# Kernel tuning notes

Measured on AMD Instinct MI355X. Metric: run time of the kernel, lower is better.

The kernel has to match this reference:

```python
import jax, jax.numpy as jnp
import numpy as np


def sparsemax(z):
    """Euclidean projection onto the simplex (Martins & Astudillo 2016).
    z: (..., L) logits -> sparse probability vectors of same shape.
    """
    L = z.shape[-1]
    z_sorted = jnp.flip(jnp.sort(z, axis=-1), axis=-1)          # descending
    cum = jnp.cumsum(z_sorted, axis=-1)
    k = jnp.arange(1, L + 1, dtype=z.dtype)                     # 1..L
    support = 1.0 + k * z_sorted > cum                          # prefix-true mask
    k_max = jnp.sum(support, axis=-1, keepdims=True).astype(z.dtype)
    # sum of z_sorted over the support == cumsum at the last supported index
    cum_at_k = jnp.sum(jnp.where(support, z_sorted, 0.0), axis=-1, keepdims=True)
    tau = (cum_at_k - 1.0) / k_max
    return jnp.maximum(z - tau, 0.0)


def setup_inputs() -> dict:
    key = jax.random.key(0)
    k1, k2 = jax.random.split(key)
    B, K, L = 64, 16, 16384
    attention_logits = jax.random.normal(k1, (B, K, L), dtype=jnp.float32)
    rationale_mask = (jax.random.uniform(k2, (B, L)) < 0.1).astype(jnp.float32)
    return {"attention_logits": attention_logits, "rationale_mask": rationale_mask}


def reference(attention_logits, rationale_mask):
    # normalize the rationale mask into a probability target q
    q = rationale_mask / jnp.clip(
        jnp.sum(rationale_mask, axis=-1, keepdims=True), 1e-12, None
    )  # (B, L)
    p = sparsemax(attention_logits)            # (B, K, L), all heads batched
    diff = p - q[:, None, :]                   # broadcast target over heads
    # per-(example, head) loss 0.5*||p - q||^2, then mean over batch and heads
    # (= mean over heads of per-head batch means, as in the torch loop)
    return 0.5 * jnp.mean(jnp.sum(diff * diff, axis=-1))
```

## Files before the change

### kernel.cpp

```cpp
#include <hip/hip_runtime.h>

#define BB 64
#define KK 16
#define LL 16384
#define CAP 2048

__global__ __launch_bounds__(256) void mask_stats_kernel(
    const float* __restrict__ mask, float* __restrict__ stats) {
  int b = blockIdx.x;
  const float* m = mask + (size_t)b * LL;
  int t = threadIdx.x;
  float s = 0.f, sq = 0.f;
#pragma unroll
  for (int j = 0; j < 16; ++j) {
    float4 v = reinterpret_cast<const float4*>(m)[j * 256 + t];
    s  += v.x + v.y + v.z + v.w;
    sq += v.x * v.x + v.y * v.y + v.z * v.z + v.w * v.w;
  }
  for (int off = 32; off; off >>= 1) {
    s  += __shfl_xor(s, off);
    sq += __shfl_xor(sq, off);
  }
  __shared__ float ls[4], lsq[4];
  int wave = t >> 6;
  if ((t & 63) == 0) { ls[wave] = s; lsq[wave] = sq; }
  __syncthreads();
  if (t == 0) {
    float S  = ls[0] + ls[1] + ls[2] + ls[3];
    float SQ = lsq[0] + lsq[1] + lsq[2] + lsq[3];
    float inv = 1.0f / fmaxf(S, 1e-12f);
    stats[2 * b]     = inv;
    stats[2 * b + 1] = SQ * inv * inv;
  }
}

__global__ __launch_bounds__(256) void sparsemax_loss_kernel(
    const float* __restrict__ logits, const float* __restrict__ mask,
    const float* __restrict__ stats, float* __restrict__ out) {
  int row = blockIdx.x;
  int b = row >> 4;
  const float* z = logits + (size_t)row * LL;
  const float* m = mask + (size_t)b * LL;
  int t = threadIdx.x;
  int wave = t >> 6, lane = t & 63;

  __shared__ float lds_val[CAP];
  __shared__ int   lds_idx[CAP];
  __shared__ int   lds_n;
  __shared__ float lds_f[4];

  if (t == 0) lds_n = 0;

  float4 v[16];
  float vmax = -3.0e38f;
#pragma unroll
  for (int j = 0; j < 16; ++j) {
    v[j] = reinterpret_cast<const float4*>(z)[j * 256 + t];
    vmax = fmaxf(vmax, fmaxf(fmaxf(v[j].x, v[j].y), fmaxf(v[j].z, v[j].w)));
  }
  for (int off = 32; off; off >>= 1) vmax = fmaxf(vmax, __shfl_xor(vmax, off));
  if (lane == 0) lds_f[wave] = vmax;
  __syncthreads();
  float zmax = fmaxf(fmaxf(lds_f[0], lds_f[1]), fmaxf(lds_f[2], lds_f[3]));
  float thr = zmax - 1.0f;

#pragma unroll
  for (int j = 0; j < 16; ++j) {
    int base = (j * 256 + t) * 4;
    float vv[4] = {v[j].x, v[j].y, v[j].z, v[j].w};
#pragma unroll
    for (int e = 0; e < 4; ++e) {
      if (vv[e] > thr) {
        int pos = atomicAdd(&lds_n, 1);
        if (pos < CAP) { lds_val[pos] = vv[e]; lds_idx[pos] = base + e; }
      }
    }
  }
  __syncthreads();
  int n = lds_n;
  float inv_s = stats[2 * b];
  float sumq2 = stats[2 * b + 1];
  const float scale = 0.5f / (float)(BB * KK);

  if (n <= 64) {
    if (wave == 0) {
      float c = (lane < n) ? lds_val[lane] : -3.0e38f;
#pragma unroll
      for (int size = 2; size <= 64; size <<= 1) {
#pragma unroll
        for (int stride = size >> 1; stride > 0; stride >>= 1) {
          float other = __shfl_xor(c, stride);
          bool dirDesc = ((lane & size) == 0);
          bool takeMax = (dirDesc == ((lane & stride) == 0));
          float mn = fminf(c, other), mx = fmaxf(c, other);
          c = takeMax ? mx : mn;
        }
      }
      float cum = c;
#pragma unroll
      for (int off = 1; off < 64; off <<= 1) {
        float y = __shfl_up(cum, off);
        if (lane >= off) cum += y;
      }
      bool sup = (lane < n) && (1.0f + (float)(lane + 1) * c > cum);
      unsigned long long bal = __ballot(sup);
      int k = __popcll(bal);
      float S = sup ? c : 0.f;
      for (int off = 32; off; off >>= 1) S += __shfl_xor(S, off);
      float tau = (S - 1.0f) / (float)k;

      float a1 = 0.f, a2 = 0.f;
      if (lane < n) {
        float val = lds_val[lane];
        float p = fmaxf(val - tau, 0.f);
        if (p > 0.f) {
          float q = m[lds_idx[lane]] * inv_s;
          a1 = p * p;
          a2 = p * q;
        }
      }
      for (int off = 32; off; off >>= 1) {
        a1 += __shfl_xor(a1, off);
        a2 += __shfl_xor(a2, off);
      }
      if (lane == 0) atomicAdd(out, (a1 - 2.f * a2 + sumq2) * scale);
    }
  } else if (n <= CAP) {
    if (wave == 0) {
      int nj = (n + 63) >> 6;
      float lo = thr, hi = zmax;
      for (int it = 0; it < 30; ++it) {
        float mid = 0.5f * (lo + hi);
        float s = 0.f;
        for (int j = 0; j < nj; ++j) {
          int i = j * 64 + lane;
          float cc = (i < n) ? lds_val[i] : -3.0e38f;
          s += fmaxf(cc - mid, 0.f);
        }
        for (int off = 32; off; off >>= 1) s += __shfl_xor(s, off);
        if (s >= 1.0f) lo = mid; else hi = mid;
      }
      float S = 0.f, kc = 0.f;
      for (int j = 0; j < nj; ++j) {
        int i = j * 64 + lane;
        float cc = (i < n) ? lds_val[i] : -3.0e38f;
        if (cc > lo) { S += cc; kc += 1.f; }
      }
      for (int off = 32; off; off >>= 1) {
        S  += __shfl_xor(S, off);
        kc += __shfl_xor(kc, off);
      }
      float tau = (S - 1.0f) / kc;

      float a1 = 0.f, a2 = 0.f;
      for (int j = 0; j < nj; ++j) {
        int i = j * 64 + lane;
        if (i < n) {
          float p = fmaxf(lds_val[i] - tau, 0.f);
          if (p > 0.f) {
            float q = m[lds_idx[i]] * inv_s;
            a1 += p * p;
            a2 += p * q;
          }
        }
      }
      for (int off = 32; off; off >>= 1) {
        a1 += __shfl_xor(a1, off);
        a2 += __shfl_xor(a2, off);
      }
      if (lane == 0) atomicAdd(out, (a1 - 2.f * a2 + sumq2) * scale);
    }
  } else {
    __shared__ float red[4], red2[4];
    float lo = thr, hi = zmax;
    for (int it = 0; it < 30; ++it) {
      float mid = 0.5f * (lo + hi);
      float s = 0.f;
      for (int j = 0; j < 16; ++j) {
        float4 vv = reinterpret_cast<const float4*>(z)[j * 256 + t];
        s += fmaxf(vv.x - mid, 0.f) + fmaxf(vv.y - mid, 0.f) +
             fmaxf(vv.z - mid, 0.f) + fmaxf(vv.w - mid, 0.f);
      }
      for (int off = 32; off; off >>= 1) s += __shfl_xor(s, off);
      __syncthreads();
      if (lane == 0) red[wave] = s;
      __syncthreads();
      float tot = red[0] + red[1] + red[2] + red[3];
      if (tot >= 1.0f) lo = mid; else hi = mid;
    }
    float S = 0.f, kc = 0.f;
    for (int j = 0; j < 16; ++j) {
      float4 vv4 = reinterpret_cast<const float4*>(z)[j * 256 + t];
      float vv[4] = {vv4.x, vv4.y, vv4.z, vv4.w};
      for (int e = 0; e < 4; ++e)
        if (vv[e] > lo) { S += vv[e]; kc += 1.f; }
    }
    for (int off = 32; off; off >>= 1) {
      S  += __shfl_xor(S, off);
      kc += __shfl_xor(kc, off);
    }
    __syncthreads();
    if (lane == 0) { red[wave] = S; red2[wave] = kc; }
    __syncthreads();
    S  = red[0] + red[1] + red[2] + red[3];
    kc = red2[0] + red2[1] + red2[2] + red2[3];
    float tau = (S - 1.0f) / kc;

    float a1 = 0.f, a2 = 0.f;
    for (int j = 0; j < 16; ++j) {
      int base = (j * 256 + t) * 4;
      float4 vv4 = reinterpret_cast<const float4*>(z)[j * 256 + t];
      float vv[4] = {vv4.x, vv4.y, vv4.z, vv4.w};
      for (int e = 0; e < 4; ++e) {
        float p = fmaxf(vv[e] - tau, 0.f);
        if (p > 0.f) {
          float q = m[base + e] * inv_s;
          a1 += p * p;
          a2 += p * q;
        }
      }
    }
    for (int off = 32; off; off >>= 1) {
      a1 += __shfl_xor(a1, off);
      a2 += __shfl_xor(a2, off);
    }
    __syncthreads();
    if (lane == 0) { red[wave] = a1; red2[wave] = a2; }
    __syncthreads();
    if (t == 0) {
      a1 = red[0] + red[1] + red[2] + red[3];
      a2 = red2[0] + red2[1] + red2[2] + red2[3];
      atomicAdd(out, (a1 - 2.f * a2 + sumq2) * scale);
    }
  }
}

extern "C" void kernel_launch(void* const* d_in, const int* in_sizes, int n_in,
                              void* d_out, int out_size, void* d_ws, size_t ws_size,
                              hipStream_t stream) {
  const float* logits = (const float*)d_in[0];
  const float* mask   = (const float*)d_in[1];
  float* stats = (float*)d_ws;
  float* out   = (float*)d_out;

  hipMemsetAsync(out, 0, sizeof(float), stream);
  mask_stats_kernel<<<BB, 256, 0, stream>>>(mask, stats);
  sparsemax_loss_kernel<<<BB * KK, 256, 0, stream>>>(logits, mask, stats, out);
}
```

Before: 111.0 us.

## Split rows into segments across three kernels for rowmax, compaction, and solve

Restructures the single per-row kernel into three passes: a segmented row-max kernel, which also computes the mask stats, using atomicMax on order-preserving keys; a segmented compaction kernel writing candidates to global memory; and a wave-per-row solve kernel. The goal is more blocks for parallelism and latency hiding on the 64MB logits read. In exchange, logits are now read twice from global memory, and it adds extra launches, a memset, and global atomics on per-row counters.

```diff
diff --git a/kernel.cpp b/kernel.cpp
--- a/kernel.cpp
+++ b/kernel.cpp
@@ -3,236 +3,199 @@
 #define BB 64
 #define KK 16
 #define LL 16384
-#define CAP 2048
-
-__global__ __launch_bounds__(256) void mask_stats_kernel(
-    const float* __restrict__ mask, float* __restrict__ stats) {
-  int b = blockIdx.x;
+#define NROW (BB * KK)
+#define SEGS 4
+#define CAP 512
+
+__device__ __forceinline__ unsigned fkey(float f) {
+  unsigned u = __float_as_uint(f);
+  return (u & 0x80000000u) ? ~u : (u | 0x80000000u);
+}
+__device__ __forceinline__ float funkey(unsigned k) {
+  unsigned u = (k & 0x80000000u) ? (k & 0x7fffffffu) : ~k;
+  return __uint_as_float(u);
+}
+
+__global__ __launch_bounds__(256) void k1_rowmax_maskstats(
+    const float* __restrict__ logits, const float* __restrict__ mask,
+    unsigned* __restrict__ rowmax, float* __restrict__ stats) {
+  int gb = blockIdx.x, t = threadIdx.x, wave = t >> 6, lane = t & 63;
+  __shared__ float l0[4], l1[4];
+  if (gb < NROW * SEGS) {
+    int row = gb >> 2, seg = gb & 3;
+    const float4* zv = reinterpret_cast<const float4*>(logits) +
+                       (size_t)row * (LL / 4) + seg * (LL / 4 / SEGS);
+    float4 a = zv[t], b4 = zv[t + 256], c = zv[t + 512], d = zv[t + 768];
+    float m0 = fmaxf(fmaxf(a.x, a.y), fmaxf(a.z, a.w));
+    float m1 = fmaxf(fmaxf(b4.x, b4.y), fmaxf(b4.z, b4.w));
+    float m2 = fmaxf(fmaxf(c.x, c.y), fmaxf(c.z, c.w));
+    float m3 = fmaxf(fmaxf(d.x, d.y), fmaxf(d.z, d.w));
+    float m = fmaxf(fmaxf(m0, m1), fmaxf(m2, m3));
+    for (int off = 32; off; off >>= 1) m = fmaxf(m, __shfl_xor(m, off));
+    if (lane == 0) l0[wave] = m;
+    __syncthreads();
+    if (t == 0) {
+      float bm = fmaxf(fmaxf(l0[0], l0[1]), fmaxf(l0[2], l0[3]));
+      atomicMax(&rowmax[row], fkey(bm));
+    }
+  } else {
+    int b = gb - NROW * SEGS;
+    const float* m = mask + (size_t)b * LL;
+    float s = 0.f, sq = 0.f;
+#pragma unroll
+    for (int j = 0; j < 16; ++j) {
+      float4 v = reinterpret_cast<const float4*>(m)[j * 256 + t];
+      s  += v.x + v.y + v.z + v.w;
+      sq += v.x * v.x + v.y * v.y + v.z * v.z + v.w * v.w;
+    }
+    for (int off = 32; off; off >>= 1) {
+      s += __shfl_xor(s, off); sq += __shfl_xor(sq, off);
+    }
+    if (lane == 0) { l0[wave] = s; l1[wave] = sq; }
+    __syncthreads();
+    if (t == 0) {
+      float S  = l0[0] + l0[1] + l0[2] + l0[3];
+      float SQ = l1[0] + l1[1] + l1[2] + l1[3];
+      float inv = 1.0f / fmaxf(S, 1e-12f);
+      stats[2 * b]     = inv;
+      stats[2 * b + 1] = SQ * inv * inv;
+    }
+  }
+}
+
+__global__ __launch_bounds__(256) void k2_compact(
+    const float* __restrict__ logits, const unsigned* __restrict__ rowmax,
+    int* __restrict__ cnt, float* __restrict__ cval, int* __restrict__ cidx) {
+  int gb = blockIdx.x;
+  int row = gb >> 2, seg = gb & 3;
+  int t = threadIdx.x;
+  float thr = funkey(rowmax[row]) - 1.0f;
+  const float4* zv = reinterpret_cast<const float4*>(logits) +
+                     (size_t)row * (LL / 4) + seg * (LL / 4 / SEGS);
+  float4 a = zv[t], b4 = zv[t + 256], c = zv[t + 512], d = zv[t + 768];
+  int ebase = seg * (LL / SEGS);
+  float vv[16] = {a.x,  a.y,  a.z,  a.w,  b4.x, b4.y, b4.z, b4.w,
+                  c.x,  c.y,  c.z,  c.w,  d.x,  d.y,  d.z,  d.w};
+  float* cv = cval + (size_t)row * CAP;
+  int*   ci = cidx + (size_t)row * CAP;
+#pragma unroll
+  for (int j = 0; j < 16; ++j) {
+    if (vv[j] > thr) {
+      int idx = ebase + (j >> 2) * 1024 + t * 4 + (j & 3);
+      int pos = atomicAdd(&cnt[row], 1);
+      if (pos < CAP) { cv[pos] = vv[j]; ci[pos] = idx; }
+    }
+  }
+}
+
+__global__ __launch_bounds__(256) void k3_solve(
+    const float* __restrict__ logits, const float* __restrict__ mask,
+    const unsigned* __restrict__ rowmax, const int* __restrict__ cnt,
+    const float* __restrict__ cval, const int* __restrict__ cidx,
+    const float* __restrict__ stats, float* __restrict__ out) {
+  int t = threadIdx.x, wave = t >> 6, lane = t & 63;
+  int row = blockIdx.x * 4 + wave;
+  int b = row >> 4;
+  __shared__ float part[4];
+  int n = cnt[row];
+  float zmax = funkey(rowmax[row]);
+  float thr = zmax - 1.0f;
+  float inv_s = stats[2 * b], sumq2 = stats[2 * b + 1];
+  const float scale = 0.5f / (float)(BB * KK);
   const float* m = mask + (size_t)b * LL;
-  int t = threadIdx.x;
-  float s = 0.f, sq = 0.f;
-#pragma unroll
-  for (int j = 0; j < 16; ++j) {
-    float4 v = reinterpret_cast<const float4*>(m)[j * 256 + t];
-    s  += v.x + v.y + v.z + v.w;
-    sq += v.x * v.x + v.y * v.y + v.z * v.z + v.w * v.w;
-  }
-  for (int off = 32; off; off >>= 1) {
-    s  += __shfl_xor(s, off);
-    sq += __shfl_xor(sq, off);
-  }
-  __shared__ float ls[4], lsq[4];
-  int wave = t >> 6;
-  if ((t & 63) == 0) { ls[wave] = s; lsq[wave] = sq; }
-  __syncthreads();
-  if (t == 0) {
-    float S  = ls[0] + ls[1] + ls[2] + ls[3];
-    float SQ = lsq[0] + lsq[1] + lsq[2] + lsq[3];
-    float inv = 1.0f / fmaxf(S, 1e-12f);
-    stats[2 * b]     = inv;
-    stats[2 * b + 1] = SQ * inv * inv;
-  }
-}
-
-__global__ __launch_bounds__(256) void sparsemax_loss_kernel(
-    const float* __restrict__ logits, const float* __restrict__ mask,
-    const float* __restrict__ stats, float* __restrict__ out) {
-  int row = blockIdx.x;
-  int b = row >> 4;
-  const float* z = logits + (size_t)row * LL;
-  const float* m = mask + (size_t)b * LL;
-  int t = threadIdx.x;
-  int wave = t >> 6, lane = t & 63;
-
-  __shared__ float lds_val[CAP];
-  __shared__ int   lds_idx[CAP];
-  __shared__ int   lds_n;
-  __shared__ float lds_f[4];
-
-  if (t == 0) lds_n = 0;
-
-  float4 v[16];
-  float vmax = -3.0e38f;
-#pragma unroll
-  for (int j = 0; j < 16; ++j) {
-    v[j] = reinterpret_cast<const float4*>(z)[j * 256 + t];
-    vmax = fmaxf(vmax, fmaxf(fmaxf(v[j].x, v[j].y), fmaxf(v[j].z, v[j].w)));
-  }
-  for (int off = 32; off; off >>= 1) vmax = fmaxf(vmax, __shfl_xor(vmax, off));
-  if (lane == 0) lds_f[wave] = vmax;
-  __syncthreads();
-  float zmax = fmaxf(fmaxf(lds_f[0], lds_f[1]), fmaxf(lds_f[2], lds_f[3]));
-  float thr = zmax - 1.0f;
-
-#pragma unroll
-  for (int j = 0; j < 16; ++j) {
-    int base = (j * 256 + t) * 4;
-    float vv[4] = {v[j].x, v[j].y, v[j].z, v[j].w};
-#pragma unroll
-    for (int e = 0; e < 4; ++e) {
-      if (vv[e] > thr) {
-        int pos = atomicAdd(&lds_n, 1);
-        if (pos < CAP) { lds_val[pos] = vv[e]; lds_idx[pos] = base + e; }
+  const float* cv = cval + (size_t)row * CAP;
+  const int*   ci = cidx + (size_t)row * CAP;
+  float a1 = 0.f, a2 = 0.f;
+
+  if (n <= 64) {
+    float c = (lane < n) ? cv[lane] : -3.0e38f;
+#pragma unroll
+    for (int size = 2; size <= 64; size <<= 1) {
+#pragma unroll
+      for (int stride = size >> 1; stride > 0; stride >>= 1) {
+        float other = __shfl_xor(c, stride);
+        bool dirDesc = ((lane & size) == 0);
+        bool takeMax = (dirDesc == ((lane & stride) == 0));
+        c = takeMax ? fmaxf(c, other) : fminf(c, other);
       }
     }
-  }
-  __syncthreads();
-  int n = lds_n;
-  float inv_s = stats[2 * b];
-  float sumq2 = stats[2 * b + 1];
-  const float scale = 0.5f / (float)(BB * KK);
-
-  if (n <= 64) {
-    if (wave == 0) {
-      float c = (lane < n) ? lds_val[lane] : -3.0e38f;
-#pragma unroll
-      for (int size = 2; size <= 64; size <<= 1) {
-#pragma unroll
-        for (int stride = size >> 1; stride > 0; stride >>= 1) {
-          float other = __shfl_xor(c, stride);
-          bool dirDesc = ((lane & size) == 0);
-          bool takeMax = (dirDesc == ((lane & stride) == 0));
-          float mn = fminf(c, other), mx = fmaxf(c, other);
-          c = takeMax ? mx : mn;
-        }
-      }
-      float cum = c;
-#pragma unroll
-      for (int off = 1; off < 64; off <<= 1) {
-        float y = __shfl_up(cum, off);
-        if (lane >= off) cum += y;
-      }
-      bool sup = (lane < n) && (1.0f + (float)(lane + 1) * c > cum);
-      unsigned long long bal = __ballot(sup);
-      int k = __popcll(bal);
-      float S = sup ? c : 0.f;
-      for (int off = 32; off; off >>= 1) S += __shfl_xor(S, off);
-      float tau = (S - 1.0f) / (float)k;
-
-      float a1 = 0.f, a2 = 0.f;
-      if (lane < n) {
-        float val = lds_val[lane];
-        float p = fmaxf(val - tau, 0.f);
-        if (p > 0.f) {
-          float q = m[lds_idx[lane]] * inv_s;
-          a1 = p * p;
-          a2 = p * q;
-        }
-      }
-      for (int off = 32; off; off >>= 1) {
-        a1 += __shfl_xor(a1, off);
-        a2 += __shfl_xor(a2, off);
-      }
-      if (lane == 0) atomicAdd(out, (a1 - 2.f * a2 + sumq2) * scale);
+    float cum = c;
+#pragma unroll
+    for (int off = 1; off < 64; off <<= 1) {
+      float y = __shfl_up(cum, off);
+      if (lane >= off) cum += y;
+    }
+    bool sup = (lane < n) && (1.0f + (float)(lane + 1) * c > cum);
+    unsigned long long bal = __ballot(sup);
+    int k = __popcll(bal);
+    float S = sup ? c : 0.f;
+    for (int off = 32; off; off >>= 1) S += __shfl_xor(S, off);
+    float tau = (S - 1.0f) / (float)k;
+    if (lane < n) {
+      float val = cv[lane];
+      float p = fmaxf(val - tau, 0.f);
+      if (p > 0.f) { float q = m[ci[lane]] * inv_s; a1 = p * p; a2 = p * q; }
     }
   } else if (n <= CAP) {
-    if (wave == 0) {
-      int nj = (n + 63) >> 6;
-      float lo = thr, hi = zmax;
-      for (int it = 0; it < 30; ++it) {
-        float mid = 0.5f * (lo + hi);
-        float s = 0.f;
-        for (int j = 0; j < nj; ++j) {
-          int i = j * 64 + lane;
-          float cc = (i < n) ? lds_val[i] : -3.0e38f;
-          s += fmaxf(cc - mid, 0.f);
-        }
-        for (int off = 32; off; off >>= 1) s += __shfl_xor(s, off);
-        if (s >= 1.0f) lo = mid; else hi = mid;
-      }
-      float S = 0.f, kc = 0.f;
+    int nj = (n + 63) >> 6;
+    float lo = thr, hi = zmax;
+    for (int it = 0; it < 30; ++it) {
+      float mid = 0.5f * (lo + hi), s = 0.f;
       for (int j = 0; j < nj; ++j) {
         int i = j * 64 + lane;
-        float cc = (i < n) ? lds_val[i] : -3.0e38f;
-        if (cc > lo) { S += cc; kc += 1.f; }
+        float cc = (i < n) ? cv[i] : -3.0e38f;
+        s += fmaxf(cc - mid, 0.f);
       }
-      for (int off = 32; off; off >>= 1) {
-        S  += __shfl_xor(S, off);
-        kc += __shfl_xor(kc, off);
+      for (int off = 32; off; off >>= 1) s += __shfl_xor(s, off);
+      if (s >= 1.0f) lo = mid; else hi = mid;
+    }
+    float S = 0.f, kc = 0.f;
+    for (int j = 0; j < nj; ++j) {
+      int i = j * 64 + lane;
+      float cc = (i < n) ? cv[i] : -3.0e38f;
+      if (cc > lo) { S += cc; kc += 1.f; }
+    }
+    for (int off = 32; off; off >>= 1) {
+      S += __shfl_xor(S, off); kc += __shfl_xor(kc, off);
+    }
+    float tau = (S - 1.0f) / kc;
+    for (int j = 0; j < nj; ++j) {
+      int i = j * 64 + lane;
+      if (i < n) {
+        float p = fmaxf(cv[i] - tau, 0.f);
+        if (p > 0.f) { float q = m[ci[i]] * inv_s; a1 += p * p; a2 += p * q; }
       }
-      float tau = (S - 1.0f) / kc;
-
-      float a1 = 0.f, a2 = 0.f;
-      for (int j = 0; j < nj; ++j) {
-        int i = j * 64 + lane;
-        if (i < n) {
-          float p = fmaxf(lds_val[i] - tau, 0.f);
-          if (p > 0.f) {
-            float q = m[lds_idx[i]] * inv_s;
-            a1 += p * p;
-            a2 += p * q;
-          }
-        }
-      }
-      for (int off = 32; off; off >>= 1) {
-        a1 += __shfl_xor(a1, off);
-        a2 += __shfl_xor(a2, off);
-      }
-      if (lane == 0) atomicAdd(out, (a1 - 2.f * a2 + sumq2) * scale);
     }
   } else {
-    __shared__ float red[4], red2[4];
+    const float* z = logits + (size_t)row * LL;
     float lo = thr, hi = zmax;
     for (int it = 0; it < 30; ++it) {
-      float mid = 0.5f * (lo + hi);
-      float s = 0.f;
-      for (int j = 0; j < 16; ++j) {
-        float4 vv = reinterpret_cast<const float4*>(z)[j * 256 + t];
-        s += fmaxf(vv.x - mid, 0.f) + fmaxf(vv.y - mid, 0.f) +
-             fmaxf(vv.z - mid, 0.f) + fmaxf(vv.w - mid, 0.f);
-      }
+      float mid = 0.5f * (lo + hi), s = 0.f;
+      for (int i = lane; i < LL; i += 64) s += fmaxf(z[i] - mid, 0.f);
       for (int off = 32; off; off >>= 1) s += __shfl_xor(s, off);
-      __syncthreads();
-      if (lane == 0) red[wave] = s;
-      __syncthreads();
-      float tot = red[0] + red[1] + red[2] + red[3];
-      if (tot >= 1.0f) lo = mid; else hi = mid;
+      if (s >= 1.0f) lo = mid; else hi = mid;
     }
     float S = 0.f, kc = 0.f;
-    for (int j = 0; j < 16; ++j) {
-      float4 vv4 = reinterpret_cast<const float4*>(z)[j * 256 + t];
-      float vv[4] = {vv4.x, vv4.y, vv4.z, vv4.w};
-      for (int e = 0; e < 4; ++e)
-        if (vv[e] > lo) { S += vv[e]; kc += 1.f; }
+    for (int i = lane; i < LL; i += 64) {
+      float zi = z[i];
+      if (zi > lo) { S += zi; kc += 1.f; }
     }
     for (int off = 32; off; off >>= 1) {
-      S  += __shfl_xor(S, off);
-      kc += __shfl_xor(kc, off);
-    }
-    __syncthreads();
-    if (lane == 0) { red[wave] = S; red2[wave] = kc; }
-    __syncthreads();
-    S  = red[0] + red[1] + red[2] + red[3];
-    kc = red2[0] + red2[1] + red2[2] + red2[3];
+      S += __shfl_xor(S, off); kc += __shfl_xor(kc, off);
+    }
     float tau = (S - 1.0f) / kc;
-
-    float a1 = 0.f, a2 = 0.f;
-    for (int j = 0; j < 16; ++j) {
-      int base = (j * 256 + t) * 4;
-      float4 vv4 = reinterpret_cast<const float4*>(z)[j * 256 + t];
-      float vv[4] = {vv4.x, vv4.y, vv4.z, vv4.w};
-      for (int e = 0; e < 4; ++e) {
-        float p = fmaxf(vv[e] - tau, 0.f);
-        if (p > 0.f) {
-          float q = m[base + e] * inv_s;
-          a1 += p * p;
-          a2 += p * q;
-        }
-      }
-    }
-    for (int off = 32; off; off >>= 1) {
-      a1 += __shfl_xor(a1, off);
-      a2 += __shfl_xor(a2, off);
-    }
-    __syncthreads();
-    if (lane == 0) { red[wave] = a1; red2[wave] = a2; }
-    __syncthreads();
-    if (t == 0) {
-      a1 = red[0] + red[1] + red[2] + red[3];
-      a2 = red2[0] + red2[1] + red2[2] + red2[3];
-      atomicAdd(out, (a1 - 2.f * a2 + sumq2) * scale);
-    }
-  }
+    for (int i = lane; i < LL; i += 64) {
+      float p = fmaxf(z[i] - tau, 0.f);
+      if (p > 0.f) { float q = m[i] * inv_s; a1 += p * p; a2 += p * q; }
+    }
+  }
+
+  for (int off = 32; off; off >>= 1) {
+    a1 += __shfl_xor(a1, off); a2 += __shfl_xor(a2, off);
+  }
+  if (lane == 0) part[wave] = (a1 - 2.f * a2 + sumq2) * scale;
+  __syncthreads();
+  if (t == 0) atomicAdd(out, part[0] + part[1] + part[2] + part[3]);
 }
 
 extern "C" void kernel_launch(void* const* d_in, const int* in_sizes, int n_in,
@@ -240,10 +203,17 @@
                               hipStream_t stream) {
   const float* logits = (const float*)d_in[0];
   const float* mask   = (const float*)d_in[1];
-  float* stats = (float*)d_ws;
-  float* out   = (float*)d_out;
+  char* ws = (char*)d_ws;
+  float*    stats  = (float*)ws;
+  unsigned* rowmax = (unsigned*)(ws + 512);
+  int*      cnt    = (int*)(ws + 512 + 4096);
+  float*    cval   = (float*)(ws + 16384);
+  int*      cidx   = (int*)(ws + 16384 + (size_t)NROW * CAP * 4);
+  float* out = (float*)d_out;
 
   hipMemsetAsync(out, 0, sizeof(float), stream);
-  mask_stats_kernel<<<BB, 256, 0, stream>>>(mask, stats);
-  sparsemax_loss_kernel<<<BB * KK, 256, 0, stream>>>(logits, mask, stats, out);
-}
+  hipMemsetAsync(ws + 512, 0, 8192, stream);
+  k1_rowmax_maskstats<<<NROW * SEGS + BB, 256, 0, stream>>>(logits, mask, rowmax, stats);
+  k2_compact<<<NROW * SEGS, 256, 0, stream>>>(logits, rowmax, cnt, cval, cidx);
+  k3_solve<<<NROW / 4, 256, 0, stream>>>(logits, mask, rowmax, cnt, cval, cidx, stats, out);
+}
```

Result: slower. 139.5 us (+25.7%).

## Stage logits row in LDS via async global_load_lds instead of registers

Applied to the files above, without the earlier changes.

Each row's logits are now loaded with async global-to-LDS loads into a 60KB shared buffer, plus one float4 tail per thread kept in registers. This frees the 64-register float4 array so two blocks can fit per CU (launch_bounds 256,2), aiming for more memory-level parallelism. The candidate buffer shrinks from 2048 to 256 entries, so rows with more than 256 candidates take the slow full-row bisection path, which now reads from LDS rather than re-reading global memory. LDS usage of about 63KB per block may limit occupancy to the intended two blocks.

```diff
diff --git a/kernel.cpp b/kernel.cpp
--- a/kernel.cpp
+++ b/kernel.cpp
@@ -3,7 +3,20 @@
 #define BB 64
 #define KK 16
 #define LL 16384
-#define CAP 2048
+#define NROW (BB * KK)
+#define NCHUNK 60
+#define CHUNKS_PER_WAVE 15
+#define LDSF (NCHUNK * 256)
+#define TAILB LDSF
+#define CAPL 256
+
+#define AS1 __attribute__((address_space(1)))
+#define AS3 __attribute__((address_space(3)))
+
+__device__ __forceinline__ void async_load16(const float* g, float* l) {
+  __builtin_amdgcn_global_load_lds((const AS1 unsigned int*)g,
+                                   (AS3 unsigned int*)l, 16, 0, 0);
+}
 
 __global__ __launch_bounds__(256) void mask_stats_kernel(
     const float* __restrict__ mask, float* __restrict__ stats) {
@@ -18,8 +31,7 @@
     sq += v.x * v.x + v.y * v.y + v.z * v.z + v.w * v.w;
   }
   for (int off = 32; off; off >>= 1) {
-    s  += __shfl_xor(s, off);
-    sq += __shfl_xor(sq, off);
+    s += __shfl_xor(s, off); sq += __shfl_xor(sq, off);
   }
   __shared__ float ls[4], lsq[4];
   int wave = t >> 6;
@@ -34,57 +46,76 @@
   }
 }
 
-__global__ __launch_bounds__(256) void sparsemax_loss_kernel(
+__global__ __launch_bounds__(256, 2) void sparsemax_loss_kernel(
     const float* __restrict__ logits, const float* __restrict__ mask,
     const float* __restrict__ stats, float* __restrict__ out) {
   int row = blockIdx.x;
   int b = row >> 4;
   const float* z = logits + (size_t)row * LL;
   const float* m = mask + (size_t)b * LL;
-  int t = threadIdx.x;
-  int wave = t >> 6, lane = t & 63;
-
-  __shared__ float lds_val[CAP];
-  __shared__ int   lds_idx[CAP];
+  int t = threadIdx.x, wave = t >> 6, lane = t & 63;
+
+  __shared__ float zrow[LDSF];
+  __shared__ float cand_v[CAPL];
+  __shared__ int   cand_i[CAPL];
+  __shared__ float lds_f[4], red0[4], red1[4];
   __shared__ int   lds_n;
-  __shared__ float lds_f[4];
 
   if (t == 0) lds_n = 0;
 
-  float4 v[16];
-  float vmax = -3.0e38f;
-#pragma unroll
-  for (int j = 0; j < 16; ++j) {
-    v[j] = reinterpret_cast<const float4*>(z)[j * 256 + t];
-    vmax = fmaxf(vmax, fmaxf(fmaxf(v[j].x, v[j].y), fmaxf(v[j].z, v[j].w)));
-  }
-  for (int off = 32; off; off >>= 1) vmax = fmaxf(vmax, __shfl_xor(vmax, off));
-  if (lane == 0) lds_f[wave] = vmax;
+#pragma unroll
+  for (int j = 0; j < CHUNKS_PER_WAVE; ++j) {
+    int c = wave * CHUNKS_PER_WAVE + j;
+    async_load16(z + c * 256 + lane * 4, &zrow[c * 256]);
+  }
+  float4 tail = reinterpret_cast<const float4*>(z)[TAILB / 4 + t];
+  __syncthreads();
+
+  const float4* zl = reinterpret_cast<const float4*>(zrow);
+  float mx = fmaxf(fmaxf(tail.x, tail.y), fmaxf(tail.z, tail.w));
+#pragma unroll
+  for (int j = 0; j < 15; ++j) {
+    float4 a = zl[j * 256 + t];
+    mx = fmaxf(mx, fmaxf(fmaxf(a.x, a.y), fmaxf(a.z, a.w)));
+  }
+  for (int off = 32; off; off >>= 1) mx = fmaxf(mx, __shfl_xor(mx, off));
+  if (lane == 0) lds_f[wave] = mx;
   __syncthreads();
   float zmax = fmaxf(fmaxf(lds_f[0], lds_f[1]), fmaxf(lds_f[2], lds_f[3]));
   float thr = zmax - 1.0f;
 
 #pragma unroll
-  for (int j = 0; j < 16; ++j) {
+  for (int j = 0; j < 15; ++j) {
+    float4 a = zl[j * 256 + t];
     int base = (j * 256 + t) * 4;
-    float vv[4] = {v[j].x, v[j].y, v[j].z, v[j].w};
+    float vv[4] = {a.x, a.y, a.z, a.w};
 #pragma unroll
     for (int e = 0; e < 4; ++e) {
       if (vv[e] > thr) {
         int pos = atomicAdd(&lds_n, 1);
-        if (pos < CAP) { lds_val[pos] = vv[e]; lds_idx[pos] = base + e; }
+        if (pos < CAPL) { cand_v[pos] = vv[e]; cand_i[pos] = base + e; }
+      }
+    }
+  }
+  {
+    int base = TAILB + t * 4;
+    float vv[4] = {tail.x, tail.y, tail.z, tail.w};
+#pragma unroll
+    for (int e = 0; e < 4; ++e) {
+      if (vv[e] > thr) {
+        int pos = atomicAdd(&lds_n, 1);
+        if (pos < CAPL) { cand_v[pos] = vv[e]; cand_i[pos] = base + e; }
       }
     }
   }
   __syncthreads();
   int n = lds_n;
-  float inv_s = stats[2 * b];
-  float sumq2 = stats[2 * b + 1];
+  float inv_s = stats[2 * b], sumq2 = stats[2 * b + 1];
   const float scale = 0.5f / (float)(BB * KK);
 
   if (n <= 64) {
     if (wave == 0) {
-      float c = (lane < n) ? lds_val[lane] : -3.0e38f;
+      float c = (lane < n) ? cand_v[lane] : -3.0e38f;
 #pragma unroll
       for (int size = 2; size <= 64; size <<= 1) {
 #pragma unroll
@@ -92,8 +123,7 @@
           float other = __shfl_xor(c, stride);
           bool dirDesc = ((lane & size) == 0);
           bool takeMax = (dirDesc == ((lane & stride) == 0));
-          float mn = fminf(c, other), mx = fmaxf(c, other);
-          c = takeMax ? mx : mn;
+          c = takeMax ? fmaxf(c, other) : fminf(c, other);
         }
       }
       float cum = c;
@@ -111,30 +141,24 @@
 
       float a1 = 0.f, a2 = 0.f;
       if (lane < n) {
-        float val = lds_val[lane];
+        float val = cand_v[lane];
         float p = fmaxf(val - tau, 0.f);
-        if (p > 0.f) {
-          float q = m[lds_idx[lane]] * inv_s;
-          a1 = p * p;
-          a2 = p * q;
-        }
+        if (p > 0.f) { float q = m[cand_i[lane]] * inv_s; a1 = p * p; a2 = p * q; }
       }
       for (int off = 32; off; off >>= 1) {
-        a1 += __shfl_xor(a1, off);
-        a2 += __shfl_xor(a2, off);
+        a1 += __shfl_xor(a1, off); a2 += __shfl_xor(a2, off);
       }
       if (lane == 0) atomicAdd(out, (a1 - 2.f * a2 + sumq2) * scale);
     }
-  } else if (n <= CAP) {
+  } else if (n <= CAPL) {
     if (wave == 0) {
       int nj = (n + 63) >> 6;
       float lo = thr, hi = zmax;
       for (int it = 0; it < 30; ++it) {
-        float mid = 0.5f * (lo + hi);
-        float s = 0.f;
+        float mid = 0.5f * (lo + hi), s = 0.f;
         for (int j = 0; j < nj; ++j) {
           int i = j * 64 + lane;
-          float cc = (i < n) ? lds_val[i] : -3.0e38f;
+          float cc = (i < n) ? cand_v[i] : -3.0e38f;
           s += fmaxf(cc - mid, 0.f);
         }
         for (int off = 32; off; off >>= 1) s += __shfl_xor(s, off);
@@ -143,93 +167,91 @@
       float S = 0.f, kc = 0.f;
       for (int j = 0; j < nj; ++j) {
         int i = j * 64 + lane;
-        float cc = (i < n) ? lds_val[i] : -3.0e38f;
+        float cc = (i < n) ? cand_v[i] : -3.0e38f;
         if (cc > lo) { S += cc; kc += 1.f; }
       }
       for (int off = 32; off; off >>= 1) {
-        S  += __shfl_xor(S, off);
-        kc += __shfl_xor(kc, off);
+        S += __shfl_xor(S, off); kc += __shfl_xor(kc, off);
       }
       float tau = (S - 1.0f) / kc;
-
       float a1 = 0.f, a2 = 0.f;
       for (int j = 0; j < nj; ++j) {
         int i = j * 64 + lane;
         if (i < n) {
-          float p = fmaxf(lds_val[i] - tau, 0.f);
-          if (p > 0.f) {
-            float q = m[lds_idx[i]] * inv_s;
-            a1 += p * p;
-            a2 += p * q;
-          }
+          float p = fmaxf(cand_v[i] - tau, 0.f);
+          if (p > 0.f) { float q = m[cand_i[i]] * inv_s; a1 += p * p; a2 += p * q; }
         }
       }
       for (int off = 32; off; off >>= 1) {
-        a1 += __shfl_xor(a1, off);
-        a2 += __shfl_xor(a2, off);
+        a1 += __shfl_xor(a1, off); a2 += __shfl_xor(a2, off);
       }
       if (lane == 0) atomicAdd(out, (a1 - 2.f * a2 + sumq2) * scale);
     }
   } else {
-    __shared__ float red[4], red2[4];
     float lo = thr, hi = zmax;
     for (int it = 0; it < 30; ++it) {
       float mid = 0.5f * (lo + hi);
-      float s = 0.f;
-      for (int j = 0; j < 16; ++j) {
-        float4 vv = reinterpret_cast<const float4*>(z)[j * 256 + t];
-        s += fmaxf(vv.x - mid, 0.f) + fmaxf(vv.y - mid, 0.f) +
-             fmaxf(vv.z - mid, 0.f) + fmaxf(vv.w - mid, 0.f);
+      float s = fmaxf(tail.x - mid, 0.f) + fmaxf(tail.y - mid, 0.f) +
+                fmaxf(tail.z - mid, 0.f) + fmaxf(tail.w - mid, 0.f);
+      for (int j = 0; j < 15; ++j) {
+        float4 a = zl[j * 256 + t];
+        s += fmaxf(a.x - mid, 0.f) + fmaxf(a.y - mid, 0.f) +
+             fmaxf(a.z - mid, 0.f) + fmaxf(a.w - mid, 0.f);
       }
       for (int off = 32; off; off >>= 1) s += __shfl_xor(s, off);
       __syncthreads();
-      if (lane == 0) red[wave] = s;
+      if (lane == 0) red0[wave] = s;
       __syncthreads();
-      float tot = red[0] + red[1] + red[2] + red[3];
+      float tot = red0[0] + red0[1] + red0[2] + red0[3];
       if (tot >= 1.0f) lo = mid; else hi = mid;
     }
     float S = 0.f, kc = 0.f;
-    for (int j = 0; j < 16; ++j) {
-      float4 vv4 = reinterpret_cast<const float4*>(z)[j * 256 + t];
-      float vv[4] = {vv4.x, vv4.y, vv4.z, vv4.w};
-      for (int e = 0; e < 4; ++e)
-        if (vv[e] > lo) { S += vv[e]; kc += 1.f; }
+    {
+      float vv[4] = {tail.x, tail.y, tail.z, tail.w};
+      for (int e = 0; e < 4; ++e) if (vv[e] > lo) { S += vv[e]; kc += 1.f; }
+    }
+    for (int j = 0; j < 15; ++j) {
+      float4 a = zl[j * 256 + t];
+      float vv[4] = {a.x, a.y, a.z, a.w};
+      for (int e = 0; e < 4; ++e) if (vv[e] > lo) { S += vv[e]; kc += 1.f; }
     }
     for (int off = 32; off; off >>= 1) {
-      S  += __shfl_xor(S, off);
-      kc += __shfl_xor(kc, off);
-    }
-    __syncthreads();
-    if (lane == 0) { red[wave] = S; red2[wave] = kc; }
-    __syncthreads();
-    S  = red[0] + red[1] + red[2] + red[3];
-    kc = red2[0] + red2[1] + red2[2] + red2[3];
+      S += __shfl_xor(S, off); kc += __shfl_xor(kc, off);
+    }
+    __syncthreads();
+    if (lane == 0) { red0[wave] = S; red1[wave] = kc; }
+    __syncthreads();
+    S  = red0[0] + red0[1] + red0[2] + red0[3];
+    kc = red1[0] + red1[1] + red1[2] + red1[3];
     float tau = (S - 1.0f) / kc;
 
     float a1 = 0.f, a2 = 0.f;
-    for (int j = 0; j < 16; ++j) {
+    for (int j = 0; j < 15; ++j) {
+      float4 a = zl[j * 256 + t];
       int base = (j * 256 + t) * 4;
-      float4 vv4 = reinterpret_cast<const float4*>(z)[j * 256 + t];
-      float vv[4] = {vv4.x, vv4.y, vv4.z, vv4.w};
+      float vv[4] = {a.x, a.y, a.z, a.w};
       for (int e = 0; e < 4; ++e) {
         float p = fmaxf(vv[e] - tau, 0.f);
-        if (p > 0.f) {
-          float q = m[base + e] * inv_s;
-          a1 += p * p;
-          a2 += p * q;
-        }
+        if (p > 0.f) { float q = m[base + e] * inv_s; a1 += p * p; a2 += p * q; }
+      }
+    }
+    {
+      int base = TAILB + t * 4;
+      float vv[4] = {tail.x, tail.y, tail.z, tail.w};
+      for (int e = 0; e < 4; ++e) {
+        float p = fmaxf(vv[e] - tau, 0.f);
+        if (p > 0.f) { float q = m[base + e] * inv_s; a1 += p * p; a2 += p * q; }
       }
     }
     for (int off = 32; off; off >>= 1) {
-      a1 += __shfl_xor(a1, off);
-      a2 += __shfl_xor(a2, off);
-    }
-    __syncthreads();
-    if (lane == 0) { red[wave] = a1; red2[wave] = a2; }
+      a1 += __shfl_xor(a1, off); a2 += __shfl_xor(a2, off);
+    }
+    __syncthreads();
+    if (lane == 0) { red0[wave] = a1; red1[wave] = a2; }
     __syncthreads();
     if (t == 0) {
-      a1 = red[0] + red[1] + red[2] + red[3];
-      a2 = red2[0] + red2[1] + red2[2] + red2[3];
+      a1 = red0[0] + red0[1] + red0[2] + red0[3];
+      a2 = red1[0] + red1[1] + red1[2] + red1[3];
       atomicAdd(out, (a1 - 2.f * a2 + sumq2) * scale);
     }
   }
@@ -245,5 +267,5 @@
 
   hipMemsetAsync(out, 0, sizeof(float), stream);
   mask_stats_kernel<<<BB, 256, 0, stream>>>(mask, stats);
-  sparsemax_loss_kernel<<<BB * KK, 256, 0, stream>>>(logits, mask, stats, out);
-}
+  sparsemax_loss_kernel<<<NROW, 256, 0, stream>>>(logits, mask, stats, out);
+}
```

New measurement: 117.4 us. +5.8%, slower.
